# Optimization experiments

Measured on AMD Instinct MI355X. Metric: run time of the kernel, lower is better.

The kernel has to match this reference:

```python
import jax, jax.numpy as jnp
import numpy as np

NUM_HEADS = 16

def setup_inputs() -> dict:
    key = jax.random.key(0)
    ks = jax.random.split(key, 5)
    B, S, H = 16, 1025, 1024
    std = 0.02
    return {
        "hidden_states": jax.random.normal(ks[0], (B, S, H), jnp.float32),
        "w_qkv": jax.random.normal(ks[1], (3 * H, H), jnp.float32) * std,
        "b_qkv": jax.random.normal(ks[2], (3 * H,), jnp.float32) * std,
        "w_dense": jax.random.normal(ks[3], (H, H), jnp.float32) * std,
        "b_dense": jax.random.normal(ks[4], (H,), jnp.float32) * std,
    }

def reference(hidden_states, w_qkv, b_qkv, w_dense, b_dense):
    B, S, H = hidden_states.shape
    nh = NUM_HEADS
    hd = H // nh
    scale = hd ** -0.5
    # fused QKV projection: [B,S,3H]
    mixed = jnp.einsum('bsh,oh->bso', hidden_states, w_qkv) + b_qkv
    # reshape per torch: (B,S,nh,3,hd) -> permute(3,0,2,1,4)
    mixed = mixed.reshape(B, S, nh, 3, hd).transpose(3, 0, 2, 1, 4)
    q, k, v = mixed[0], mixed[1], mixed[2]          # each [B,nh,S,hd]
    scores = jnp.einsum('bhqd,bhkd->bhqk', q, k) * scale
    probs = jax.nn.softmax(scores, axis=-1)          # [B,nh,S,S]
    ctx = jnp.einsum('bhqk,bhkd->bhqd', probs, v)    # [B,nh,S,hd]
    ctx = ctx.transpose(0, 2, 1, 3).reshape(B, S, H)
    out = jnp.einsum('bsh,oh->bso', ctx, w_dense) + b_dense
    return out
```

## Files before the change

### kernel.cpp

```cpp
#include <hip/hip_runtime.h>
#include <math.h>

typedef float f32x4 __attribute__((ext_vector_type(4)));
typedef __bf16 bf16x8 __attribute__((ext_vector_type(8)));
typedef unsigned int u32;
typedef u32 u32x4 __attribute__((ext_vector_type(4)));

#define AS1 __attribute__((address_space(1)))
#define AS3 __attribute__((address_space(3)))

static __device__ __forceinline__ void gload16(const void* g, void* l) {
    __builtin_amdgcn_global_load_lds((const AS1 u32*)g, (AS3 u32*)l, 16, 0, 0);
}
static __device__ __forceinline__ f32x4 mfma16(bf16x8 a, bf16x8 b, f32x4 c) {
    return __builtin_amdgcn_mfma_f32_16x16x32_bf16(a, b, c, 0, 0, 0);
}
static __device__ __forceinline__ float exp2fast(float x) {
    return __builtin_amdgcn_exp2f(x);
}

__global__ __launch_bounds__(256)
void convert3_kernel(const float* __restrict__ in0, __bf16* __restrict__ out0, int nb0,
                     const float* __restrict__ in1, __bf16* __restrict__ out1, int nb1,
                     const float* __restrict__ in2, __bf16* __restrict__ out2)
{
    int b = blockIdx.x;
    const float* in; __bf16* out;
    if (b < nb0)            { in = in0; out = out0; }
    else if (b < nb0 + nb1) { in = in1; out = out1; b -= nb0; }
    else                    { in = in2; out = out2; b -= nb0 + nb1; }
    const size_t i = ((size_t)b * 256 + threadIdx.x) * 8;
    f32x4 a = *(const f32x4*)(in + i);
    f32x4 c = *(const f32x4*)(in + i + 4);
    bf16x8 o;
    #pragma unroll
    for (int j = 0; j < 4; ++j) { o[j] = (__bf16)a[j]; o[j + 4] = (__bf16)c[j]; }
    *(bf16x8*)(out + i) = o;
}

__global__ __launch_bounds__(256)
void gemm_qkv(const __bf16* __restrict__ A, const __bf16* __restrict__ Bw,
              const float* __restrict__ bias, __bf16* __restrict__ qkv)
{
    constexpr int M = 16400;
    constexpr int K = 1024;
    constexpr int NT = 24 * 129;

    __shared__ __align__(16) __bf16 As[128 * 64];
    __shared__ __align__(16) __bf16 Bs[128 * 64];

    const int tid  = threadIdx.x;
    const int lane = tid & 63;
    const int wv   = tid >> 6;
    const int wr   = wv >> 1, wc = wv & 1;
    const int fr   = lane & 15, fq = lane >> 4;

    const int xx = blockIdx.x & 7, jj = blockIdx.x >> 3;
    const int tile = xx * (NT / 8) + jj;
    const int by = tile / 24, bx = tile % 24;
    const int m0 = by * 128, n0 = bx * 128;

    const __bf16* aptr[4];
    const __bf16* bptr[4];
    int loff[4];
    #pragma unroll
    for (int qd = 0; qd < 4; ++qd) {
        const int s  = qd * 256 + tid;
        const int r  = s >> 3;
        const int c  = (s & 7) ^ (r & 7);
        loff[qd] = s * 8;
        int ar = m0 + r; if (ar > M - 1) ar = M - 1;
        aptr[qd] = A  + (size_t)ar * K + c * 8;
        bptr[qd] = Bw + (size_t)(n0 + r) * K + c * 8;
    }

    f32x4 acc[4][4];
    #pragma unroll
    for (int i = 0; i < 4; ++i)
        #pragma unroll
        for (int j = 0; j < 4; ++j)
            acc[i][j] = f32x4{0.f, 0.f, 0.f, 0.f};

    for (int kt = 0; kt < K / 64; ++kt) {
        const int kof = kt * 64;
        #pragma unroll
        for (int qd = 0; qd < 4; ++qd) {
            gload16(aptr[qd] + kof, &As[loff[qd]]);
            gload16(bptr[qd] + kof, &Bs[loff[qd]]);
        }
        __syncthreads();

        #pragma unroll
        for (int ks = 0; ks < 2; ++ks) {
            bf16x8 a[4], b[4];
            #pragma unroll
            for (int i = 0; i < 4; ++i) {
                const int ra = wr * 64 + i * 16 + fr;
                const int rb = wc * 64 + i * 16 + fr;
                const int cg = ((ks * 4 + fq) ^ (fr & 7)) * 8;
                a[i] = *(const bf16x8*)&As[ra * 64 + cg];
                b[i] = *(const bf16x8*)&Bs[rb * 64 + cg];
            }
            #pragma unroll
            for (int i = 0; i < 4; ++i)
                #pragma unroll
                for (int j = 0; j < 4; ++j)
                    acc[i][j] = mfma16(a[i], b[j], acc[i][j]);
        }
        __syncthreads();
    }

    #pragma unroll
    for (int ni = 0; ni < 4; ++ni) {
        const int col = n0 + wc * 64 + ni * 16 + fr;
        const float bv = bias[col];
        const float scale = ((col % 192) < 64) ? 0.18033688011112042f : 1.0f;
        #pragma unroll
        for (int mi = 0; mi < 4; ++mi) {
            #pragma unroll
            for (int j = 0; j < 4; ++j) {
                const int m = m0 + wr * 64 + mi * 16 + fq * 4 + j;
                if (m < M)
                    qkv[(size_t)m * 3072 + col] = (__bf16)((acc[mi][ni][j] + bv) * scale);
            }
        }
    }
}

__global__ __launch_bounds__(256)
void gemm_dense128(const __bf16* __restrict__ A, const __bf16* __restrict__ Bw,
                   const float* __restrict__ bias, float* __restrict__ f_out)
{
    constexpr int M = 16400;
    constexpr int K = 1024;

    __shared__ __align__(16) __bf16 As[128 * 64];
    __shared__ __align__(16) __bf16 Bs[128 * 64];

    const int tid  = threadIdx.x;
    const int lane = tid & 63;
    const int wv   = tid >> 6;
    const int wr   = wv >> 1, wc = wv & 1;
    const int fr   = lane & 15, fq = lane >> 4;

    const int xx = blockIdx.x & 7, jj = blockIdx.x >> 3;
    const int tile = xx * 129 + jj;
    const int m0 = (tile >> 3) * 128;
    const int n0 = (tile & 7) * 128;

    const __bf16* aptr[4];
    const __bf16* bptr[4];
    int loff[4];
    #pragma unroll
    for (int qd = 0; qd < 4; ++qd) {
        const int s  = qd * 256 + tid;
        const int r  = s >> 3;
        const int c  = (s & 7) ^ (r & 7);
        loff[qd] = s * 8;
        int ar = m0 + r; if (ar > M - 1) ar = M - 1;
        aptr[qd] = A  + (size_t)ar * K + c * 8;
        bptr[qd] = Bw + (size_t)(n0 + r) * K + c * 8;
    }

    f32x4 acc[4][4];
    #pragma unroll
    for (int i = 0; i < 4; ++i)
        #pragma unroll
        for (int j = 0; j < 4; ++j)
            acc[i][j] = f32x4{0.f, 0.f, 0.f, 0.f};

    for (int kt = 0; kt < K / 64; ++kt) {
        const int kof = kt * 64;
        #pragma unroll
        for (int qd = 0; qd < 4; ++qd) {
            gload16(aptr[qd] + kof, &As[loff[qd]]);
            gload16(bptr[qd] + kof, &Bs[loff[qd]]);
        }
        __syncthreads();

        #pragma unroll
        for (int ks = 0; ks < 2; ++ks) {
            bf16x8 a[4], b[4];
            #pragma unroll
            for (int i = 0; i < 4; ++i) {
                const int ra = wr * 64 + i * 16 + fr;
                const int rb = wc * 64 + i * 16 + fr;
                const int cg = ((ks * 4 + fq) ^ (fr & 7)) * 8;
                a[i] = *(const bf16x8*)&As[ra * 64 + cg];
                b[i] = *(const bf16x8*)&Bs[rb * 64 + cg];
            }
            #pragma unroll
            for (int i = 0; i < 4; ++i)
                #pragma unroll
                for (int j = 0; j < 4; ++j)
                    acc[i][j] = mfma16(a[i], b[j], acc[i][j]);
        }
        __syncthreads();
    }

    #pragma unroll
    for (int ni = 0; ni < 4; ++ni) {
        const int col = n0 + wc * 64 + ni * 16 + fr;
        const float bv = bias[col];
        #pragma unroll
        for (int mi = 0; mi < 4; ++mi) {
            #pragma unroll
            for (int j = 0; j < 4; ++j) {
                const int m = m0 + wr * 64 + mi * 16 + fq * 4 + j;
                if (m < M) f_out[(size_t)m * 1024 + col] = acc[mi][ni][j] + bv;
            }
        }
    }
}

__global__ __launch_bounds__(256)
void transpose_v(const __bf16* __restrict__ qkvb, __bf16* __restrict__ vt)
{
    constexpr int S = 1025, S2 = 1088;
    const int bh = blockIdx.y;
    const int bb = bh >> 4, hh = bh & 15;
    const int s0 = blockIdx.x * 64;
    const int sr = threadIdx.x >> 2, sq = threadIdx.x & 3;
    int srow = s0 + sr; if (srow > S - 1) srow = S - 1;
    const __bf16* src = qkvb + ((size_t)(bb * 1025) + srow) * 3072
                             + hh * 192 + 128 + sq * 16;
    bf16x8 v0 = *(const bf16x8*)src;
    bf16x8 v1 = *(const bf16x8*)(src + 8);
    __bf16* dst = vt + (size_t)bh * 64 * S2 + s0 + sr;
    #pragma unroll
    for (int i = 0; i < 8; ++i) {
        dst[(size_t)(sq * 16 + i) * S2]     = v0[i];
        dst[(size_t)(sq * 16 + 8 + i) * S2] = v1[i];
    }
}

__global__ __launch_bounds__(512)
void attn_kernel(const __bf16* __restrict__ qkvb, const __bf16* __restrict__ vtb,
                 __bf16* __restrict__ ctxb)
{
    constexpr int S = 1025, S2 = 1088, ROW = 3072;
    const int tid  = threadIdx.x;
    const int lane = tid & 63;
    const int w    = tid >> 6;
    const int fr   = lane & 15, fq = lane >> 4;

    const int xx = blockIdx.x & 7, jj = blockIdx.x >> 3;
    const int tile = xx * 288 + jj;
    const int bh = tile / 9;
    const int q0 = (tile % 9) * 128;
    const int bb = bh >> 4, hh = bh & 15;

    const __bf16* qp = qkvb + (size_t)(bb * 1025) * ROW + hh * 192;
    const __bf16* kp = qp + 64;
    const __bf16* vp = vtb + (size_t)bh * 64 * S2;

    __shared__ __align__(16) __bf16 Ks[64 * 64];
    __shared__ __align__(16) __bf16 Vs[64 * 64];
    __shared__ u32 Ps[8][16 * 33];

    const int r0 = tid >> 3, g0 = (tid & 7) ^ ((tid >> 3) & 7);

    int qrow = q0 + w * 16 + fr; if (qrow > S - 1) qrow = S - 1;
    const bf16x8 qa0 = *(const bf16x8*)(qp + (size_t)qrow * ROW + fq * 8);
    const bf16x8 qa1 = *(const bf16x8*)(qp + (size_t)qrow * ROW + 32 + fq * 8);

    f32x4 ctx[4];
    #pragma unroll
    for (int di = 0; di < 4; ++di) ctx[di] = f32x4{0.f, 0.f, 0.f, 0.f};
    float mrow = -1e30f;
    float lrow = 0.f;

    u32* psrow_w = &Ps[w][fr * 33];

    for (int kt = 0; kt < 17; ++kt) {
        const int kv0 = kt * 64;
        {
            int kr = kv0 + r0; if (kr > S - 1) kr = S - 1;
            gload16(kp + (size_t)kr * ROW + g0 * 8, &Ks[tid * 8]);
            gload16(vp + (size_t)r0 * S2 + kv0 + g0 * 8, &Vs[tid * 8]);
        }
        __syncthreads();

        f32x4 sc[4];
        #pragma unroll
        for (int ni = 0; ni < 4; ++ni) {
            const int row = ni * 16 + fr;
            bf16x8 kf0 = *(const bf16x8*)&Ks[row * 64 + ((fq    ) ^ (row & 7)) * 8];
            bf16x8 kf1 = *(const bf16x8*)&Ks[row * 64 + ((fq + 4) ^ (row & 7)) * 8];
            f32x4 z = f32x4{0.f, 0.f, 0.f, 0.f};
            z = mfma16(kf0, qa0, z);
            sc[ni] = mfma16(kf1, qa1, z);
        }
        if (kv0 + 64 > S) {
            #pragma unroll
            for (int ni = 0; ni < 4; ++ni)
                #pragma unroll
                for (int j = 0; j < 4; ++j)
                    if (kv0 + ni * 16 + fq * 4 + j >= S) sc[ni][j] = -1e30f;
        }

        float mt = sc[0][0];
        #pragma unroll
        for (int ni = 0; ni < 4; ++ni)
            #pragma unroll
            for (int j = 0; j < 4; ++j) mt = fmaxf(mt, sc[ni][j]);
        mt = fmaxf(mt, __shfl_xor(mt, 16, 64));
        mt = fmaxf(mt, __shfl_xor(mt, 32, 64));

        if (__any(mt > mrow + 8.0f)) {
            const float mnew = fmaxf(mrow, mt);
            const float alpha = exp2fast(mrow - mnew);
            mrow = mnew;
            lrow *= alpha;
            float av[4];
            #pragma unroll
            for (int j = 0; j < 4; ++j) av[j] = __shfl(alpha, fq * 4 + j, 64);
            #pragma unroll
            for (int di = 0; di < 4; ++di) {
                ctx[di][0] *= av[0]; ctx[di][1] *= av[1];
                ctx[di][2] *= av[2]; ctx[di][3] *= av[3];
            }
        }

        float p[4][4];
        float s = 0.f;
        #pragma unroll
        for (int ni = 0; ni < 4; ++ni)
            #pragma unroll
            for (int j = 0; j < 4; ++j) {
                p[ni][j] = exp2fast(sc[ni][j] - mrow);
                s += p[ni][j];
            }
        s += __shfl_xor(s, 16, 64);
        s += __shfl_xor(s, 32, 64);
        lrow += s;

        #pragma unroll
        for (int ni = 0; ni < 4; ++ni) {
            #pragma unroll
            for (int h = 0; h < 2; ++h) {
                unsigned short lo = __builtin_bit_cast(unsigned short, (__bf16)p[ni][2 * h]);
                unsigned short hi = __builtin_bit_cast(unsigned short, (__bf16)p[ni][2 * h + 1]);
                psrow_w[fq * 8 + ni * 2 + h] = (u32)lo | ((u32)hi << 16);
            }
        }
        u32x4 pav[2];
        #pragma unroll
        for (int ks = 0; ks < 2; ++ks)
            #pragma unroll
            for (int t = 0; t < 4; ++t) {
                const int slot = (2 * (fq & 1) + (t >> 1)) * 8
                               + (2 * ks + (fq >> 1)) * 2 + (t & 1);
                pav[ks][t] = psrow_w[slot];
            }

        #pragma unroll
        for (int ks = 0; ks < 2; ++ks) {
            const bf16x8 pa = __builtin_bit_cast(bf16x8, pav[ks]);
            #pragma unroll
            for (int di = 0; di < 4; ++di) {
                const int row = di * 16 + fr;
                bf16x8 vf = *(const bf16x8*)&Vs[row * 64 + ((ks * 4 + fq) ^ (row & 7)) * 8];
                ctx[di] = mfma16(pa, vf, ctx[di]);
            }
        }
        __syncthreads();
    }

    float linv[4];
    #pragma unroll
    for (int j = 0; j < 4; ++j) linv[j] = 1.0f / __shfl(lrow, fq * 4 + j, 64);
    #pragma unroll
    for (int di = 0; di < 4; ++di) {
        #pragma unroll
        for (int j = 0; j < 4; ++j) {
            const int qg = q0 + w * 16 + fq * 4 + j;
            if (qg < S) {
                ctxb[((size_t)bb * 1025 + qg) * 1024 + hh * 64 + di * 16 + fr] =
                    (__bf16)(ctx[di][j] * linv[j]);
            }
        }
    }
}

extern "C" void kernel_launch(void* const* d_in, const int* in_sizes, int n_in,
                              void* d_out, int out_size, void* d_ws, size_t ws_size,
                              hipStream_t stream)
{
    const float* hs      = (const float*)d_in[0];
    const float* w_qkv   = (const float*)d_in[1];
    const float* b_qkv   = (const float*)d_in[2];
    const float* w_dense = (const float*)d_in[3];
    const float* b_dense = (const float*)d_in[4];

    const size_t nHS  = (size_t)16 * 1025 * 1024;
    const size_t nWQ  = (size_t)3072 * 1024;
    const size_t nWD  = (size_t)1024 * 1024;
    const size_t nQKV = (size_t)16400 * 3072;

    __bf16* hsb     = (__bf16*)d_ws;
    __bf16* wqkvb   = hsb + nHS;
    __bf16* wdenseb = wqkvb + nWQ;
    __bf16* qkvb    = wdenseb + nWD;
    __bf16* ctxb    = qkvb + nQKV;
    __bf16* vtb     = ctxb + nHS;

    convert3_kernel<<<dim3(8200 + 1536 + 512), dim3(256), 0, stream>>>(
        hs, hsb, 8200, w_qkv, wqkvb, 1536, w_dense, wdenseb);

    gemm_qkv<<<dim3(24 * 129), dim3(256), 0, stream>>>(
        hsb, wqkvb, b_qkv, qkvb);

    transpose_v<<<dim3(17, 256), dim3(256), 0, stream>>>(qkvb, vtb);

    attn_kernel<<<dim3(8 * 288), dim3(512), 0, stream>>>(qkvb, vtb, ctxb);

    gemm_dense128<<<dim3(8 * 129), dim3(256), 0, stream>>>(
        ctxb, wdenseb, b_dense, (float*)d_out);
}
```

Before: 437.7 us.

## Enlarge GEMM tiles to 256x128 with 512-thread blocks via templated kernel

Merges the QKV and dense projection GEMMs into one templated kernel that uses 256x128 output tiles and 8 waves per block instead of 128x128 and 4 waves. Each B tile loaded into LDS is now shared by twice as many rows, which reduces global and LDS traffic per output element. The costs are more LDS per block (48KB), fewer blocks in the grid, possibly lower occupancy, and more padded rows in the last M tile, since 16400 is not a multiple of 256.

New measurement: 389.7 us. 1.12x faster.

```diff
diff --git a/kernel.cpp b/kernel.cpp
--- a/kernel.cpp
+++ b/kernel.cpp
@@ -38,40 +38,51 @@
     *(bf16x8*)(out + i) = o;
 }
 
-__global__ __launch_bounds__(256)
-void gemm_qkv(const __bf16* __restrict__ A, const __bf16* __restrict__ Bw,
-              const float* __restrict__ bias, __bf16* __restrict__ qkv)
+template<int MODE>
+__global__ __launch_bounds__(512)
+void gemm_big(const __bf16* __restrict__ A, const __bf16* __restrict__ Bw,
+              const float* __restrict__ bias, __bf16* __restrict__ qkv,
+              float* __restrict__ f_out)
 {
     constexpr int M = 16400;
     constexpr int K = 1024;
-    constexpr int NT = 24 * 129;
-
-    __shared__ __align__(16) __bf16 As[128 * 64];
+    constexpr int NBX = (MODE == 0) ? 24 : 8;
+    constexpr int NOUT = (MODE == 0) ? 3072 : 1024;
+    constexpr int CHUNK = (65 * NBX) / 8;
+
+    __shared__ __align__(16) __bf16 As[256 * 64];
     __shared__ __align__(16) __bf16 Bs[128 * 64];
 
     const int tid  = threadIdx.x;
     const int lane = tid & 63;
     const int wv   = tid >> 6;
-    const int wr   = wv >> 1, wc = wv & 1;
+    const int wrm  = wv >> 1;
+    const int wcn  = wv & 1;
     const int fr   = lane & 15, fq = lane >> 4;
 
     const int xx = blockIdx.x & 7, jj = blockIdx.x >> 3;
-    const int tile = xx * (NT / 8) + jj;
-    const int by = tile / 24, bx = tile % 24;
-    const int m0 = by * 128, n0 = bx * 128;
-
-    const __bf16* aptr[4];
-    const __bf16* bptr[4];
-    int loff[4];
+    const int tile = xx * CHUNK + jj;
+    const int by = tile / NBX, bx = tile % NBX;
+    const int m0 = by * 256, n0 = bx * 128;
+
+    const __bf16* aptr[4]; int aoff[4];
     #pragma unroll
     for (int qd = 0; qd < 4; ++qd) {
-        const int s  = qd * 256 + tid;
-        const int r  = s >> 3;
-        const int c  = (s & 7) ^ (r & 7);
-        loff[qd] = s * 8;
+        const int s = qd * 512 + tid;
+        const int r = s >> 3;
+        const int c = (s & 7) ^ (r & 7);
+        aoff[qd] = s * 8;
         int ar = m0 + r; if (ar > M - 1) ar = M - 1;
-        aptr[qd] = A  + (size_t)ar * K + c * 8;
-        bptr[qd] = Bw + (size_t)(n0 + r) * K + c * 8;
+        aptr[qd] = A + (size_t)ar * K + c * 8;
+    }
+    const __bf16* bptr[2]; int boff[2];
+    #pragma unroll
+    for (int l = 0; l < 2; ++l) {
+        const int s = l * 512 + tid;
+        const int r = s >> 3;
+        const int c = (s & 7) ^ (r & 7);
+        boff[l] = s * 8;
+        bptr[l] = Bw + (size_t)(n0 + r) * K + c * 8;
     }
 
     f32x4 acc[4][4];
@@ -84,10 +95,9 @@
     for (int kt = 0; kt < K / 64; ++kt) {
         const int kof = kt * 64;
         #pragma unroll
-        for (int qd = 0; qd < 4; ++qd) {
-            gload16(aptr[qd] + kof, &As[loff[qd]]);
-            gload16(bptr[qd] + kof, &Bs[loff[qd]]);
-        }
+        for (int qd = 0; qd < 4; ++qd) gload16(aptr[qd] + kof, &As[aoff[qd]]);
+        #pragma unroll
+        for (int l = 0; l < 2; ++l)   gload16(bptr[l] + kof, &Bs[boff[l]]);
         __syncthreads();
 
         #pragma unroll
@@ -95,11 +105,12 @@
             bf16x8 a[4], b[4];
             #pragma unroll
             for (int i = 0; i < 4; ++i) {
-                const int ra = wr * 64 + i * 16 + fr;
-                const int rb = wc * 64 + i * 16 + fr;
-                const int cg = ((ks * 4 + fq) ^ (fr & 7)) * 8;
-                a[i] = *(const bf16x8*)&As[ra * 64 + cg];
-                b[i] = *(const bf16x8*)&Bs[rb * 64 + cg];
+                const int ra = wrm * 64 + i * 16 + fr;
+                const int rb = wcn * 64 + i * 16 + fr;
+                const int cga = ((ks * 4 + fq) ^ (ra & 7)) * 8;
+                const int cgb = ((ks * 4 + fq) ^ (rb & 7)) * 8;
+                a[i] = *(const bf16x8*)&As[ra * 64 + cga];
+                b[i] = *(const bf16x8*)&Bs[rb * 64 + cgb];
             }
             #pragma unroll
             for (int i = 0; i < 4; ++i)
@@ -112,102 +123,28 @@
 
     #pragma unroll
     for (int ni = 0; ni < 4; ++ni) {
-        const int col = n0 + wc * 64 + ni * 16 + fr;
+        const int col = n0 + wcn * 64 + ni * 16 + fr;
         const float bv = bias[col];
-        const float scale = ((col % 192) < 64) ? 0.18033688011112042f : 1.0f;
-        #pragma unroll
-        for (int mi = 0; mi < 4; ++mi) {
-            #pragma unroll
-            for (int j = 0; j < 4; ++j) {
-                const int m = m0 + wr * 64 + mi * 16 + fq * 4 + j;
-                if (m < M)
-                    qkv[(size_t)m * 3072 + col] = (__bf16)((acc[mi][ni][j] + bv) * scale);
-            }
-        }
-    }
-}
-
-__global__ __launch_bounds__(256)
-void gemm_dense128(const __bf16* __restrict__ A, const __bf16* __restrict__ Bw,
-                   const float* __restrict__ bias, float* __restrict__ f_out)
-{
-    constexpr int M = 16400;
-    constexpr int K = 1024;
-
-    __shared__ __align__(16) __bf16 As[128 * 64];
-    __shared__ __align__(16) __bf16 Bs[128 * 64];
-
-    const int tid  = threadIdx.x;
-    const int lane = tid & 63;
-    const int wv   = tid >> 6;
-    const int wr   = wv >> 1, wc = wv & 1;
-    const int fr   = lane & 15, fq = lane >> 4;
-
-    const int xx = blockIdx.x & 7, jj = blockIdx.x >> 3;
-    const int tile = xx * 129 + jj;
-    const int m0 = (tile >> 3) * 128;
-    const int n0 = (tile & 7) * 128;
-
-    const __bf16* aptr[4];
-    const __bf16* bptr[4];
-    int loff[4];
-    #pragma unroll
-    for (int qd = 0; qd < 4; ++qd) {
-        const int s  = qd * 256 + tid;
-        const int r  = s >> 3;
-        const int c  = (s & 7) ^ (r & 7);
-        loff[qd] = s * 8;
-        int ar = m0 + r; if (ar > M - 1) ar = M - 1;
-        aptr[qd] = A  + (size_t)ar * K + c * 8;
-        bptr[qd] = Bw + (size_t)(n0 + r) * K + c * 8;
-    }
-
-    f32x4 acc[4][4];
-    #pragma unroll
-    for (int i = 0; i < 4; ++i)
-        #pragma unroll
-        for (int j = 0; j < 4; ++j)
-            acc[i][j] = f32x4{0.f, 0.f, 0.f, 0.f};
-
-    for (int kt = 0; kt < K / 64; ++kt) {
-        const int kof = kt * 64;
-        #pragma unroll
-        for (int qd = 0; qd < 4; ++qd) {
-            gload16(aptr[qd] + kof, &As[loff[qd]]);
-            gload16(bptr[qd] + kof, &Bs[loff[qd]]);
-        }
-        __syncthreads();
-
-        #pragma unroll
-        for (int ks = 0; ks < 2; ++ks) {
-            bf16x8 a[4], b[4];
-            #pragma unroll
-            for (int i = 0; i < 4; ++i) {
-                const int ra = wr * 64 + i * 16 + fr;
-                const int rb = wc * 64 + i * 16 + fr;
-                const int cg = ((ks * 4 + fq) ^ (fr & 7)) * 8;
-                a[i] = *(const bf16x8*)&As[ra * 64 + cg];
-                b[i] = *(const bf16x8*)&Bs[rb * 64 + cg];
-            }
-            #pragma unroll
-            for (int i = 0; i < 4; ++i)
+        if constexpr (MODE == 0) {
+            const float scale = ((col % 192) < 64) ? 0.18033688011112042f : 1.0f;
+            #pragma unroll
+            for (int mi = 0; mi < 4; ++mi) {
                 #pragma unroll
-                for (int j = 0; j < 4; ++j)
-                    acc[i][j] = mfma16(a[i], b[j], acc[i][j]);
-        }
-        __syncthreads();
-    }
-
-    #pragma unroll
-    for (int ni = 0; ni < 4; ++ni) {
-        const int col = n0 + wc * 64 + ni * 16 + fr;
-        const float bv = bias[col];
-        #pragma unroll
-        for (int mi = 0; mi < 4; ++mi) {
-            #pragma unroll
-            for (int j = 0; j < 4; ++j) {
-                const int m = m0 + wr * 64 + mi * 16 + fq * 4 + j;
-                if (m < M) f_out[(size_t)m * 1024 + col] = acc[mi][ni][j] + bv;
+                for (int j = 0; j < 4; ++j) {
+                    const int m = m0 + wrm * 64 + mi * 16 + fq * 4 + j;
+                    if (m < M)
+                        qkv[(size_t)m * NOUT + col] =
+                            (__bf16)((acc[mi][ni][j] + bv) * scale);
+                }
+            }
+        } else {
+            #pragma unroll
+            for (int mi = 0; mi < 4; ++mi) {
+                #pragma unroll
+                for (int j = 0; j < 4; ++j) {
+                    const int m = m0 + wrm * 64 + mi * 16 + fq * 4 + j;
+                    if (m < M) f_out[(size_t)m * NOUT + col] = acc[mi][ni][j] + bv;
+                }
             }
         }
     }
@@ -408,13 +345,13 @@
     convert3_kernel<<<dim3(8200 + 1536 + 512), dim3(256), 0, stream>>>(
         hs, hsb, 8200, w_qkv, wqkvb, 1536, w_dense, wdenseb);
 
-    gemm_qkv<<<dim3(24 * 129), dim3(256), 0, stream>>>(
-        hsb, wqkvb, b_qkv, qkvb);
+    gemm_big<0><<<dim3(65 * 24), dim3(512), 0, stream>>>(
+        hsb, wqkvb, b_qkv, qkvb, nullptr);
 
     transpose_v<<<dim3(17, 256), dim3(256), 0, stream>>>(qkvb, vtb);
 
     attn_kernel<<<dim3(8 * 288), dim3(512), 0, stream>>>(qkvb, vtb, ctxb);
 
-    gemm_dense128<<<dim3(8 * 129), dim3(256), 0, stream>>>(
-        ctxb, wdenseb, b_dense, (float*)d_out);
-}
+    gemm_big<1><<<dim3(65 * 8), dim3(512), 0, stream>>>(
+        ctxb, wdenseb, b_dense, nullptr, (float*)d_out);
+}
```
